# Kernel tuning notes

Measured on AMD Instinct MI355X. Metric: run time of the kernel, lower is better.

Reference implementation:

```python
import jax, jax.numpy as jnp
import numpy as np

B, H, SEQLEN, HEAD_DIM = 1, 16, 4096, 64
SCALE = 1.0 / float(np.sqrt(HEAD_DIM))


def setup_inputs() -> dict:
    key = jax.random.key(0)
    kq, kk, kv = jax.random.split(key, 3)
    q = jax.random.normal(kq, (B, H, SEQLEN, HEAD_DIM), dtype=jnp.float32)
    k = jax.random.normal(kk, (B, H, HEAD_DIM, SEQLEN), dtype=jnp.float32)  # pre-transposed
    v = jax.random.normal(kv, (B, H, SEQLEN, HEAD_DIM), dtype=jnp.float32)
    return {"q": q, "k": k, "v": v}


def reference(q, k, v):
    # causal additive mask: -inf strictly above the diagonal
    mask = jnp.where(
        jnp.triu(jnp.ones((SEQLEN, SEQLEN), dtype=bool), k=1),
        jnp.float32(-jnp.inf), jnp.float32(0.0),
    ).astype(q.dtype)
    scores = jnp.einsum('bhsd,bhdt->bhst', q, k) * SCALE + mask  # [B,H,S,S]
    row_max = jnp.max(scores, axis=-1, keepdims=True)
    p_exp = jnp.exp(scores - row_max)
    denom = jnp.sum(p_exp, axis=-1, keepdims=True)
    p = p_exp / denom                                            # softmax probs
    out = jnp.einsum('bhst,bhtd->bhsd', p, v)                    # [B,H,S,D]
    row_sum = jnp.sum(p, axis=2)                                 # per-key accumulated attention [B,H,S]
    return (out, row_sum)
```

## Files before the change

kernel.cpp:

```cpp
#include <hip/hip_runtime.h>
#include <hip/hip_bf16.h>

#define HEADS 16
#define SEQ   4096
#define DIM   64
#define QT    64
#define KT    64
#define SCALE 0.125f
#define CF    0.18033688011112042f
#define LOG2E 1.4426950408889634f

typedef __bf16 v8bf  __attribute__((ext_vector_type(8)));
typedef __bf16 v4bf  __attribute__((ext_vector_type(4)));
typedef float  f32x4 __attribute__((ext_vector_type(4)));

__device__ __forceinline__ __bf16 to_bf(float f) { return (__bf16)f; }
__device__ __forceinline__ float ex2(float x) { return __builtin_amdgcn_exp2f(x); }
__device__ __forceinline__ float lg2(float x) { return __builtin_amdgcn_logf(x); }

__device__ __forceinline__ void gload16(const __bf16* g, __bf16* l) {
    __builtin_amdgcn_global_load_lds(
        (const __attribute__((address_space(1))) void*)g,
        (__attribute__((address_space(3))) void*)l,
        16, 0, 0);
}

__global__ __launch_bounds__(256) void conv_q_kernel(
    const float* __restrict__ qg, __bf16* __restrict__ Qb)
{
    size_t i = ((size_t)blockIdx.x * 256 + threadIdx.x) * 8;
    float4 f0 = *(const float4*)(qg + i);
    float4 f1 = *(const float4*)(qg + i + 4);
    v8bf o;
    o[0] = to_bf(f0.x * CF); o[1] = to_bf(f0.y * CF);
    o[2] = to_bf(f0.z * CF); o[3] = to_bf(f0.w * CF);
    o[4] = to_bf(f1.x * CF); o[5] = to_bf(f1.y * CF);
    o[6] = to_bf(f1.z * CF); o[7] = to_bf(f1.w * CF);
    *(v8bf*)(Qb + i) = o;
}

__global__ __launch_bounds__(256) void conv_kv_kernel(
    const float* __restrict__ kg, const float* __restrict__ vg,
    __bf16* __restrict__ Kb, __bf16* __restrict__ Vb)
{
    __shared__ __bf16 ldsT[64][65];
    const int h   = blockIdx.y;
    const int t0  = blockIdx.x * 64;
    const int tid = threadIdx.x;
    const int rr  = tid >> 2;
    const int cq  = (tid & 3) * 16;

    if (blockIdx.z == 0) {
        const float* src = kg + ((size_t)h * DIM + rr) * SEQ + t0 + cq;
        #pragma unroll
        for (int j = 0; j < 4; ++j) {
            float4 f = *(const float4*)(src + 4 * j);
            ldsT[rr][cq + 4 * j + 0] = to_bf(f.x);
            ldsT[rr][cq + 4 * j + 1] = to_bf(f.y);
            ldsT[rr][cq + 4 * j + 2] = to_bf(f.z);
            ldsT[rr][cq + 4 * j + 3] = to_bf(f.w);
        }
        __syncthreads();
        __bf16* dst = Kb + (size_t)h * SEQ * DIM + (size_t)(t0 + rr) * DIM + cq;
        v8bf o0, o1;
        #pragma unroll
        for (int i = 0; i < 8; ++i) {
            o0[i] = ldsT[cq + i][rr];
            o1[i] = ldsT[cq + 8 + i][rr];
        }
        *(v8bf*)dst = o0;
        *(v8bf*)(dst + 8) = o1;
    } else {
        const float* src = vg + ((size_t)h * SEQ + t0 + rr) * DIM + cq;
        #pragma unroll
        for (int j = 0; j < 4; ++j) {
            float4 f = *(const float4*)(src + 4 * j);
            ldsT[rr][cq + 4 * j + 0] = to_bf(f.x);
            ldsT[rr][cq + 4 * j + 1] = to_bf(f.y);
            ldsT[rr][cq + 4 * j + 2] = to_bf(f.z);
            ldsT[rr][cq + 4 * j + 3] = to_bf(f.w);
        }
        __syncthreads();
        __bf16* dst0 = Vb + ((size_t)h * DIM + rr) * SEQ + t0;
        const int n  = cq >> 4;
        const int c0 = 32 * (n >> 1) + 4 * (n & 1);
        #pragma unroll
        for (int j2 = 0; j2 < 4; ++j2) {
            v4bf ch;
            #pragma unroll
            for (int r = 0; r < 4; ++r)
                ch[r] = ldsT[cq + 4 * j2 + r][rr];
            *(v4bf*)(dst0 + c0 + 8 * j2) = ch;
        }
    }
}

__global__ __launch_bounds__(256, 2) void fa_fwd2_kernel(
    const __bf16* __restrict__ Qb, const __bf16* __restrict__ Kb,
    const __bf16* __restrict__ Vb, float* __restrict__ outg,
    float* __restrict__ lseg)
{
    const int b    = blockIdx.x;
    const int xcd  = b & 7;
    const int j    = b >> 3;
    const int h    = 2 * xcd + (j & 1);
    const int bq   = j >> 1;
    const int tid  = threadIdx.x;
    const int wave = tid >> 6;
    const int lane = tid & 63;
    const int g    = lane >> 4;
    const int l16  = lane & 15;

    __shared__ alignas(16) __bf16 ldsK[2][2][KT * DIM];
    __shared__ alignas(16) __bf16 ldsV[2][2][DIM * KT];

    const int r0 = tid >> 3;
    const int c0 = tid & 7;
    const size_t kOff0 = (size_t)r0 * DIM + (size_t)((c0 ^ (r0 & 7)) << 3);
    const size_t kOff1 = (size_t)(r0 + 32) * DIM + (size_t)((c0 ^ ((r0 + 32) & 7)) << 3);
    const size_t vOff0 = (size_t)r0 * SEQ + (size_t)((c0 ^ (r0 & 7)) << 3);
    const size_t vOff1 = (size_t)(r0 + 32) * SEQ + (size_t)((c0 ^ ((r0 + 32) & 7)) << 3);
    const __bf16* KbH = Kb + (size_t)h * SEQ * DIM;
    const __bf16* VbH = Vb + (size_t)h * DIM * SEQ;
    const int ldsW = wave * 512;

    #pragma unroll 1
    for (int pi = 0; pi < 2; ++pi) {
        const int qtile = pi ? (63 - bq) : bq;
        const int qw = qtile * QT + wave * 16;
        const int nt  = qtile + 1;
        const int nIt = (nt + 1) >> 1;
        const int q   = qw + l16;

        const __bf16* qrow = Qb + ((size_t)h * SEQ + q) * DIM + g * 8;
        v8bf aq0 = *(const v8bf*)qrow;
        v8bf aq1 = *(const v8bf*)(qrow + 32);

        f32x4 acc[4];
        #pragma unroll
        for (int n = 0; n < 4; ++n) acc[n] = (f32x4){0.f, 0.f, 0.f, 0.f};
        float lp[4] = {0.f, 0.f, 0.f, 0.f};

        int cur = 0;
        #pragma unroll
        for (int u = 0; u < 2; ++u) {
            const __bf16* kb = KbH + (size_t)(64 * u) * DIM;
            const __bf16* vb = VbH + 64 * u;
            gload16(kb + kOff0, &ldsK[0][u][ldsW]);
            gload16(kb + kOff1, &ldsK[0][u][2048 + ldsW]);
            gload16(vb + vOff0, &ldsV[0][u][ldsW]);
            gload16(vb + vOff1, &ldsV[0][u][2048 + ldsW]);
        }
        __syncthreads();

        #pragma unroll 1
        for (int it = 0; it < nIt; ++it) {
            if (it + 1 < nIt) {
                #pragma unroll
                for (int u = 0; u < 2; ++u) {
                    const __bf16* kb = KbH + (size_t)(128 * (it + 1) + 64 * u) * DIM;
                    const __bf16* vb = VbH + 128 * (it + 1) + 64 * u;
                    gload16(kb + kOff0, &ldsK[cur ^ 1][u][ldsW]);
                    gload16(kb + kOff1, &ldsK[cur ^ 1][u][2048 + ldsW]);
                    gload16(vb + vOff0, &ldsV[cur ^ 1][u][ldsW]);
                    gload16(vb + vOff1, &ldsV[cur ^ 1][u][2048 + ldsW]);
                }
            }
            f32x4 s0[4], s1[4];
            #pragma unroll
            for (int n = 0; n < 4; ++n) {
                s0[n] = (f32x4){0.f, 0.f, 0.f, 0.f};
                s1[n] = (f32x4){0.f, 0.f, 0.f, 0.f};
            }
            __builtin_amdgcn_s_setprio(1);
            #pragma unroll
            for (int kk = 0; kk < 2; ++kk) {
                #pragma unroll
                for (int n = 0; n < 4; ++n) {
                    int row  = 16 * n + l16;
                    int byte = row * 128 + kk * 64 + g * 16;
                    byte ^= (row & 7) << 4;
                    v8bf ak0 = *(const v8bf*)&ldsK[cur][0][byte >> 1];
                    v8bf ak1 = *(const v8bf*)&ldsK[cur][1][byte >> 1];
                    s0[n] = __builtin_amdgcn_mfma_f32_16x16x32_bf16(
                        ak0, kk ? aq1 : aq0, s0[n], 0, 0, 0);
                    s1[n] = __builtin_amdgcn_mfma_f32_16x16x32_bf16(
                        ak1, kk ? aq1 : aq0, s1[n], 0, 0, 0);
                }
            }
            __builtin_amdgcn_s_setprio(0);
            const int st0 = 2 * it, st1 = 2 * it + 1;
            if (st0 >= nt - 1) {
                const int lim = (qtile - st0) * 64 + wave * 16 + l16;
                #pragma unroll
                for (int n = 0; n < 4; ++n)
                    #pragma unroll
                    for (int r = 0; r < 4; ++r)
                        if (16 * n + 4 * g + r > lim) s0[n][r] = -3.0e38f;
            }
            if (st1 >= nt - 1) {
                const int lim = (qtile - st1) * 64 + wave * 16 + l16;
                #pragma unroll
                for (int n = 0; n < 4; ++n)
                    #pragma unroll
                    for (int r = 0; r < 4; ++r)
                        if (16 * n + 4 * g + r > lim) s1[n][r] = -3.0e38f;
            }
            v8bf pa00, pa01, pa10, pa11;
            #pragma unroll
            for (int n = 0; n < 4; ++n) {
                #pragma unroll
                for (int r = 0; r < 4; ++r) {
                    float p0 = ex2(s0[n][r]);
                    float p1 = ex2(s1[n][r]);
                    lp[r] += p0 + p1;
                    if (n < 2) { pa00[(n & 1) * 4 + r] = to_bf(p0);
                                 pa10[(n & 1) * 4 + r] = to_bf(p1); }
                    else       { pa01[(n & 1) * 4 + r] = to_bf(p0);
                                 pa11[(n & 1) * 4 + r] = to_bf(p1); }
                }
            }
            __builtin_amdgcn_s_setprio(1);
            #pragma unroll
            for (int kk = 0; kk < 2; ++kk) {
                #pragma unroll
                for (int n = 0; n < 4; ++n) {
                    int row  = 16 * n + l16;
                    int byte = row * 128 + kk * 64 + g * 16;
                    byte ^= (row & 7) << 4;
                    v8bf av0 = *(const v8bf*)&ldsV[cur][0][byte >> 1];
                    v8bf av1 = *(const v8bf*)&ldsV[cur][1][byte >> 1];
                    acc[n] = __builtin_amdgcn_mfma_f32_16x16x32_bf16(
                        av0, kk ? pa01 : pa00, acc[n], 0, 0, 0);
                    acc[n] = __builtin_amdgcn_mfma_f32_16x16x32_bf16(
                        av1, kk ? pa11 : pa10, acc[n], 0, 0, 0);
                }
            }
            __builtin_amdgcn_s_setprio(0);
            __syncthreads();
            cur ^= 1;
        }

        float l = (lp[0] + lp[1]) + (lp[2] + lp[3]);
        l += __shfl_xor(l, 16);
        l += __shfl_xor(l, 32);
        const float inv = 1.0f / l;
        float* orow = outg + ((size_t)h * SEQ + q) * DIM;
        #pragma unroll
        for (int n = 0; n < 4; ++n) {
            f32x4 o = acc[n];
            o[0] *= inv; o[1] *= inv; o[2] *= inv; o[3] *= inv;
            *(f32x4*)(orow + 16 * n + 4 * g) = o;
        }
        if (g == 0)
            lseg[h * SEQ + q] = lg2(l);
    }
}

__global__ __launch_bounds__(256, 2) void fa_colsum2_kernel(
    const __bf16* __restrict__ Qb, const __bf16* __restrict__ Kb,
    const float* __restrict__ lseg, float* __restrict__ rsg)
{
    const int b    = blockIdx.x;
    const int xcd  = b & 7;
    const int j    = b >> 3;
    const int h    = 2 * xcd + (j & 1);
    const int ta   = j >> 1;
    const int tb   = 63 - ta;
    const int tid  = threadIdx.x;
    const int wave = tid >> 6;
    const int lane = tid & 63;
    const int g    = lane >> 4;
    const int l16  = lane & 15;

    __shared__ alignas(16) __bf16 ldsK2[2][KT * DIM];
    __shared__ float cs[2][4][KT];

    const int r0 = tid >> 3;
    const int c0 = tid & 7;
    const size_t kOff0 = (size_t)r0 * DIM + (size_t)((c0 ^ (r0 & 7)) << 3);
    const size_t kOff1 = (size_t)(r0 + 32) * DIM + (size_t)((c0 ^ ((r0 + 32) & 7)) << 3);
    const __bf16* KbH = Kb + (size_t)h * SEQ * DIM;
    const int ldsW = wave * 512;

    gload16(KbH + (size_t)ta * KT * DIM + kOff0, &ldsK2[0][ldsW]);
    gload16(KbH + (size_t)ta * KT * DIM + kOff1, &ldsK2[0][2048 + ldsW]);
    gload16(KbH + (size_t)tb * KT * DIM + kOff0, &ldsK2[1][ldsW]);
    gload16(KbH + (size_t)tb * KT * DIM + kOff1, &ldsK2[1][2048 + ldsW]);
    __syncthreads();

    float accA[4] = {0.f, 0.f, 0.f, 0.f};
    float accB[4] = {0.f, 0.f, 0.f, 0.f};

    #pragma unroll 1
    for (int qt = ta; qt < SEQ / QT; ++qt) {
        const int qw = qt * QT + wave * 16;
        const __bf16* qrow = Qb + ((size_t)h * SEQ + qw + l16) * DIM + g * 8;
        v8bf aq0 = *(const v8bf*)qrow;
        v8bf aq1 = *(const v8bf*)(qrow + 32);
        float4 lse4 = *(const float4*)(lseg + (size_t)h * SEQ + qw + 4 * g);

        {
            f32x4 s[4];
            #pragma unroll
            for (int n = 0; n < 4; ++n) s[n] = (f32x4){0.f, 0.f, 0.f, 0.f};
            __builtin_amdgcn_s_setprio(1);
            #pragma unroll
            for (int kk = 0; kk < 2; ++kk)
                #pragma unroll
                for (int n = 0; n < 4; ++n) {
                    int row  = 16 * n + l16;
                    int byte = row * 128 + kk * 64 + g * 16;
                    byte ^= (row & 7) << 4;
                    v8bf bk = *(const v8bf*)&ldsK2[0][byte >> 1];
                    s[n] = __builtin_amdgcn_mfma_f32_16x16x32_bf16(
                        kk ? aq1 : aq0, bk, s[n], 0, 0, 0);
                }
            __builtin_amdgcn_s_setprio(0);
            if (qt == ta) {
                #pragma unroll
                for (int n = 0; n < 4; ++n) {
                    const int key = ta * KT + 16 * n + l16;
                    #pragma unroll
                    for (int r = 0; r < 4; ++r) {
                        float e = ex2(s[n][r] - lse4[r]);
                        accA[n] += (key <= qw + 4 * g + r) ? e : 0.f;
                    }
                }
            } else {
                #pragma unroll
                for (int n = 0; n < 4; ++n)
                    #pragma unroll
                    for (int r = 0; r < 4; ++r)
                        accA[n] += ex2(s[n][r] - lse4[r]);
            }
        }
        if (qt >= tb) {
            f32x4 s[4];
            #pragma unroll
            for (int n = 0; n < 4; ++n) s[n] = (f32x4){0.f, 0.f, 0.f, 0.f};
            __builtin_amdgcn_s_setprio(1);
            #pragma unroll
            for (int kk = 0; kk < 2; ++kk)
                #pragma unroll
                for (int n = 0; n < 4; ++n) {
                    int row  = 16 * n + l16;
                    int byte = row * 128 + kk * 64 + g * 16;
                    byte ^= (row & 7) << 4;
                    v8bf bk = *(const v8bf*)&ldsK2[1][byte >> 1];
                    s[n] = __builtin_amdgcn_mfma_f32_16x16x32_bf16(
                        kk ? aq1 : aq0, bk, s[n], 0, 0, 0);
                }
            __builtin_amdgcn_s_setprio(0);
            if (qt == tb) {
                #pragma unroll
                for (int n = 0; n < 4; ++n) {
                    const int key = tb * KT + 16 * n + l16;
                    #pragma unroll
                    for (int r = 0; r < 4; ++r) {
                        float e = ex2(s[n][r] - lse4[r]);
                        accB[n] += (key <= qw + 4 * g + r) ? e : 0.f;
                    }
                }
            } else {
                #pragma unroll
                for (int n = 0; n < 4; ++n)
                    #pragma unroll
                    for (int r = 0; r < 4; ++r)
                        accB[n] += ex2(s[n][r] - lse4[r]);
            }
        }
    }

    #pragma unroll
    for (int n = 0; n < 4; ++n) {
        accA[n] += __shfl_xor(accA[n], 16);
        accA[n] += __shfl_xor(accA[n], 32);
        accB[n] += __shfl_xor(accB[n], 16);
        accB[n] += __shfl_xor(accB[n], 32);
    }
    if (lane < 16) {
        #pragma unroll
        for (int n = 0; n < 4; ++n) {
            cs[0][wave][16 * n + lane] = accA[n];
            cs[1][wave][16 * n + lane] = accB[n];
        }
    }
    __syncthreads();
    if (tid < KT) {
        rsg[(size_t)h * SEQ + ta * KT + tid] =
            cs[0][0][tid] + cs[0][1][tid] + cs[0][2][tid] + cs[0][3][tid];
    } else if (tid < 2 * KT) {
        const int t = tid - KT;
        rsg[(size_t)h * SEQ + tb * KT + t] =
            cs[1][0][t] + cs[1][1][t] + cs[1][2][t] + cs[1][3][t];
    }
}

__global__ __launch_bounds__(256, 1) void fa_fwd_v1_kernel(
    const float* __restrict__ qg, const float* __restrict__ kg,
    const float* __restrict__ vg, float* __restrict__ outg,
    float* __restrict__ lseg)
{
    const int h    = blockIdx.y;
    const int q0   = blockIdx.x * QT;
    const int tid  = threadIdx.x;
    const int wave = tid >> 6;
    const int lane = tid & 63;
    const int g    = lane >> 4;
    const int l16  = lane & 15;

    __shared__ alignas(16) __bf16 ldsK[KT * DIM];
    __shared__ alignas(16) __bf16 ldsV[DIM * KT];
    __shared__ alignas(16) __bf16 ldsP[4][16 * 72];

    const int qw = q0 + wave * 16;
    v8bf aq[2];
    {
        const float* qrow = qg + ((size_t)h * SEQ + qw + l16) * DIM;
        #pragma unroll
        for (int kk = 0; kk < 2; ++kk) {
            const float* p = qrow + kk * 32 + g * 8;
            float4 f0 = *(const float4*)p;
            float4 f1 = *(const float4*)(p + 4);
            aq[kk][0] = to_bf(f0.x); aq[kk][1] = to_bf(f0.y);
            aq[kk][2] = to_bf(f0.z); aq[kk][3] = to_bf(f0.w);
            aq[kk][4] = to_bf(f1.x); aq[kk][5] = to_bf(f1.y);
            aq[kk][6] = to_bf(f1.z); aq[kk][7] = to_bf(f1.w);
        }
    }
    f32x4 acc[4];
    #pragma unroll
    for (int n = 0; n < 4; ++n) acc[n] = (f32x4){0.f, 0.f, 0.f, 0.f};
    float m_r[4], l_r[4];
    #pragma unroll
    for (int r = 0; r < 4; ++r) { m_r[r] = -__builtin_inff(); l_r[r] = 0.f; }

    const int ntiles = q0 / KT + 1;
    const int kd = tid >> 2;
    const int kc = (tid & 3) * 16;

    for (int t = 0; t < ntiles; ++t) {
        const int t0 = t * KT;
        __syncthreads();
        {
            const float* src = kg + ((size_t)h * DIM + kd) * SEQ + t0 + kc;
            #pragma unroll
            for (int j = 0; j < 4; ++j) {
                float4 f = *(const float4*)(src + 4 * j);
                #pragma unroll
                for (int i = 0; i < 4; ++i) {
                    int row  = kc + 4 * j + i;
                    int byte = row * 128 + kd * 2;
                    byte ^= (row & 7) << 4;
                    ldsK[byte >> 1] = to_bf(((const float*)&f)[i]);
                }
            }
        }
        {
            const float* src = vg + ((size_t)h * SEQ + t0 + kd) * DIM + kc;
            #pragma unroll
            for (int j = 0; j < 4; ++j) {
                float4 f = *(const float4*)(src + 4 * j);
                #pragma unroll
                for (int i = 0; i < 4; ++i) {
                    int row  = kc + 4 * j + i;
                    int byte = row * 128 + kd * 2;
                    byte ^= (row & 7) << 4;
                    ldsV[byte >> 1] = to_bf(((const float*)&f)[i]);
                }
            }
        }
        __syncthreads();

        f32x4 s[4];
        #pragma unroll
        for (int n = 0; n < 4; ++n) s[n] = (f32x4){0.f, 0.f, 0.f, 0.f};
        #pragma unroll
        for (int kk = 0; kk < 2; ++kk)
            #pragma unroll
            for (int n = 0; n < 4; ++n) {
                int row  = 16 * n + l16;
                int byte = row * 128 + kk * 64 + g * 16;
                byte ^= (row & 7) << 4;
                v8bf bk = *(const v8bf*)&ldsK[byte >> 1];
                s[n] = __builtin_amdgcn_mfma_f32_16x16x32_bf16(aq[kk], bk, s[n], 0, 0, 0);
            }
        float pvv[4][4];
        #pragma unroll
        for (int r = 0; r < 4; ++r) {
            const int qq = qw + 4 * g + r;
            float sv[4];
            #pragma unroll
            for (int n = 0; n < 4; ++n) {
                int key = t0 + 16 * n + l16;
                sv[n] = (key <= qq) ? s[n][r] * (SCALE * LOG2E) : -3.0e38f;
            }
            float mx = fmaxf(fmaxf(sv[0], sv[1]), fmaxf(sv[2], sv[3]));
            mx = fmaxf(mx, __shfl_xor(mx, 1));
            mx = fmaxf(mx, __shfl_xor(mx, 2));
            mx = fmaxf(mx, __shfl_xor(mx, 4));
            mx = fmaxf(mx, __shfl_xor(mx, 8));
            float mnew = fmaxf(m_r[r], mx);
            float corr = ex2(m_r[r] - mnew);
            m_r[r] = mnew;
            float rs = 0.f;
            #pragma unroll
            for (int n = 0; n < 4; ++n) {
                float p = (sv[n] > -1.0e38f) ? ex2(sv[n] - mnew) : 0.f;
                pvv[n][r] = p;
                rs += p;
            }
            rs += __shfl_xor(rs, 1);
            rs += __shfl_xor(rs, 2);
            rs += __shfl_xor(rs, 4);
            rs += __shfl_xor(rs, 8);
            l_r[r] = l_r[r] * corr + rs;
            #pragma unroll
            for (int n = 0; n < 4; ++n) acc[n][r] *= corr;
        }
        #pragma unroll
        for (int n = 0; n < 4; ++n)
            #pragma unroll
            for (int r = 0; r < 4; ++r)
                ldsP[wave][(4 * g + r) * 72 + 16 * n + l16] = to_bf(pvv[n][r]);
        asm volatile("s_waitcnt lgkmcnt(0)" ::: "memory");
        __builtin_amdgcn_sched_barrier(0);
        #pragma unroll
        for (int kk = 0; kk < 2; ++kk) {
            v8bf ap = *(const v8bf*)&ldsP[wave][l16 * 72 + 32 * kk + 8 * g];
            #pragma unroll
            for (int n = 0; n < 4; ++n) {
                int row  = 16 * n + l16;
                int byte = row * 128 + kk * 64 + g * 16;
                byte ^= (row & 7) << 4;
                v8bf bv = *(const v8bf*)&ldsV[byte >> 1];
                acc[n] = __builtin_amdgcn_mfma_f32_16x16x32_bf16(ap, bv, acc[n], 0, 0, 0);
            }
        }
    }
    #pragma unroll
    for (int r = 0; r < 4; ++r) {
        const int qq  = qw + 4 * g + r;
        const float inv = 1.0f / l_r[r];
        float* orow = outg + ((size_t)h * SEQ + qq) * DIM;
        #pragma unroll
        for (int n = 0; n < 4; ++n)
            orow[16 * n + l16] = acc[n][r] * inv;
        if (l16 == 0)
            lseg[h * SEQ + qq] = m_r[r] + lg2(l_r[r]);
    }
}

__global__ __launch_bounds__(256, 1) void fa_colsum_v1_kernel(
    const float* __restrict__ qg, const float* __restrict__ kg,
    const float* __restrict__ lseg, float* __restrict__ rsg)
{
    const int h    = blockIdx.y;
    const int t0   = blockIdx.x * KT;
    const int tid  = threadIdx.x;
    const int wave = tid >> 6;
    const int lane = tid & 63;
    const int g    = lane >> 4;
    const int l16  = lane & 15;

    __shared__ alignas(16) __bf16 ldsK[KT * DIM];
    __shared__ float cs[4][KT];
    {
        const int kd = tid >> 2;
        const int kc = (tid & 3) * 16;
        const float* src = kg + ((size_t)h * DIM + kd) * SEQ + t0 + kc;
        #pragma unroll
        for (int j = 0; j < 4; ++j) {
            float4 f = *(const float4*)(src + 4 * j);
            #pragma unroll
            for (int i = 0; i < 4; ++i) {
                int row  = kc + 4 * j + i;
                int byte = row * 128 + kd * 2;
                byte ^= (row & 7) << 4;
                ldsK[byte >> 1] = to_bf(((const float*)&f)[i]);
            }
        }
    }
    __syncthreads();
    float colacc[4] = {0.f, 0.f, 0.f, 0.f};
    for (int qt = t0 / QT; qt < SEQ / QT; ++qt) {
        const int qw = qt * QT + wave * 16;
        const float* qrow = qg + ((size_t)h * SEQ + qw + l16) * DIM;
        v8bf aq[2];
        #pragma unroll
        for (int kk = 0; kk < 2; ++kk) {
            const float* p = qrow + kk * 32 + g * 8;
            float4 f0 = *(const float4*)p;
            float4 f1 = *(const float4*)(p + 4);
            aq[kk][0] = to_bf(f0.x); aq[kk][1] = to_bf(f0.y);
            aq[kk][2] = to_bf(f0.z); aq[kk][3] = to_bf(f0.w);
            aq[kk][4] = to_bf(f1.x); aq[kk][5] = to_bf(f1.y);
            aq[kk][6] = to_bf(f1.z); aq[kk][7] = to_bf(f1.w);
        }
        float lse_r[4];
        #pragma unroll
        for (int r = 0; r < 4; ++r)
            lse_r[r] = lseg[h * SEQ + qw + 4 * g + r];
        f32x4 s[4];
        #pragma unroll
        for (int n = 0; n < 4; ++n) s[n] = (f32x4){0.f, 0.f, 0.f, 0.f};
        #pragma unroll
        for (int kk = 0; kk < 2; ++kk)
            #pragma unroll
            for (int n = 0; n < 4; ++n) {
                int row  = 16 * n + l16;
                int byte = row * 128 + kk * 64 + g * 16;
                byte ^= (row & 7) << 4;
                v8bf bk = *(const v8bf*)&ldsK[byte >> 1];
                s[n] = __builtin_amdgcn_mfma_f32_16x16x32_bf16(aq[kk], bk, s[n], 0, 0, 0);
            }
        #pragma unroll
        for (int n = 0; n < 4; ++n) {
            const int key = t0 + 16 * n + l16;
            #pragma unroll
            for (int r = 0; r < 4; ++r) {
                const int qq = qw + 4 * g + r;
                if (key <= qq)
                    colacc[n] += ex2(s[n][r] * (SCALE * LOG2E) - lse_r[r]);
            }
        }
    }
    #pragma unroll
    for (int n = 0; n < 4; ++n) {
        colacc[n] += __shfl_xor(colacc[n], 16);
        colacc[n] += __shfl_xor(colacc[n], 32);
    }
    if (lane < 16) {
        #pragma unroll
        for (int n = 0; n < 4; ++n)
            cs[wave][16 * n + lane] = colacc[n];
    }
    __syncthreads();
    if (tid < KT) {
        float v = cs[0][tid] + cs[1][tid] + cs[2][tid] + cs[3][tid];
        rsg[h * SEQ + t0 + tid] = v;
    }
}

extern "C" void kernel_launch(void* const* d_in, const int* in_sizes, int n_in,
                              void* d_out, int out_size, void* d_ws, size_t ws_size,
                              hipStream_t stream) {
    (void)in_sizes; (void)n_in; (void)out_size;
    const float* qg = (const float*)d_in[0];
    const float* kg = (const float*)d_in[1];
    const float* vg = (const float*)d_in[2];
    float* outg = (float*)d_out;
    float* rsg  = outg + (size_t)HEADS * SEQ * DIM;

    const size_t nElem   = (size_t)HEADS * SEQ * DIM;
    const size_t lseB    = (size_t)HEADS * SEQ * sizeof(float);
    const size_t needB   = lseB + 3 * nElem * sizeof(__bf16);

    if (ws_size >= needB) {
        float*  lseg = (float*)d_ws;
        __bf16* Qb = (__bf16*)((char*)d_ws + lseB);
        __bf16* Kb = Qb + nElem;
        __bf16* Vb = Kb + nElem;
        conv_q_kernel<<<dim3((int)(nElem / 2048)), 256, 0, stream>>>(qg, Qb);
        conv_kv_kernel<<<dim3(SEQ / 64, HEADS, 2), 256, 0, stream>>>(kg, vg, Kb, Vb);
        fa_fwd2_kernel<<<dim3(512), 256, 0, stream>>>(Qb, Kb, Vb, outg, lseg);
        fa_colsum2_kernel<<<dim3(512), 256, 0, stream>>>(Qb, Kb, lseg, rsg);
    } else {
        float* lseg = (float*)d_ws;
        dim3 grid(SEQ / QT, HEADS);
        fa_fwd_v1_kernel<<<grid, 256, 0, stream>>>(qg, kg, vg, outg, lseg);
        fa_colsum_v1_kernel<<<grid, 256, 0, stream>>>(qg, kg, lseg, rsg);
    }
}
```

Baseline: 105.3 us.

## Fuse paired query tiles over shared K/V loop and split column-sum work

```diff
diff --git a/kernel.cpp b/kernel.cpp
--- a/kernel.cpp
+++ b/kernel.cpp
@@ -104,12 +104,17 @@
     const int xcd  = b & 7;
     const int j    = b >> 3;
     const int h    = 2 * xcd + (j & 1);
-    const int bq   = j >> 1;
+    const int a    = j >> 1;
     const int tid  = threadIdx.x;
     const int wave = tid >> 6;
     const int lane = tid & 63;
     const int g    = lane >> 4;
     const int l16  = lane & 15;
+    const int wit  = wave * 16 + l16;
+
+    const int na  = a + 1;
+    const int nb  = 64 - a;
+    const int nIt = (nb + 1) >> 1;
 
     __shared__ alignas(16) __bf16 ldsK[2][2][KT * DIM];
     __shared__ alignas(16) __bf16 ldsV[2][2][DIM * KT];
@@ -124,149 +129,219 @@
     const __bf16* VbH = Vb + (size_t)h * DIM * SEQ;
     const int ldsW = wave * 512;
 
+    const int qlo = a * QT + wit;
+    const int qhi = (63 - a) * QT + wit;
+
+    const __bf16* qlr = Qb + ((size_t)h * SEQ + qlo) * DIM + g * 8;
+    const __bf16* qhr = Qb + ((size_t)h * SEQ + qhi) * DIM + g * 8;
+    v8bf aqlo0 = *(const v8bf*)qlr;
+    v8bf aqlo1 = *(const v8bf*)(qlr + 32);
+    v8bf aqhi0 = *(const v8bf*)qhr;
+    v8bf aqhi1 = *(const v8bf*)(qhr + 32);
+
+    f32x4 accl[4], acch[4];
+    #pragma unroll
+    for (int n = 0; n < 4; ++n) {
+        accl[n] = (f32x4){0.f, 0.f, 0.f, 0.f};
+        acch[n] = (f32x4){0.f, 0.f, 0.f, 0.f};
+    }
+    float lpl[4] = {0.f, 0.f, 0.f, 0.f};
+    float lph[4] = {0.f, 0.f, 0.f, 0.f};
+
+    int cur = 0;
+    #pragma unroll
+    for (int u = 0; u < 2; ++u) {
+        const __bf16* kb = KbH + (size_t)(64 * u) * DIM;
+        const __bf16* vb = VbH + 64 * u;
+        gload16(kb + kOff0, &ldsK[0][u][ldsW]);
+        gload16(kb + kOff1, &ldsK[0][u][2048 + ldsW]);
+        gload16(vb + vOff0, &ldsV[0][u][ldsW]);
+        gload16(vb + vOff1, &ldsV[0][u][2048 + ldsW]);
+    }
+    __syncthreads();
+
+    auto sub_full = [&](int u, int t) {
+        f32x4 sl[4], sh[4];
+        #pragma unroll
+        for (int n = 0; n < 4; ++n) {
+            sl[n] = (f32x4){0.f, 0.f, 0.f, 0.f};
+            sh[n] = (f32x4){0.f, 0.f, 0.f, 0.f};
+        }
+        __builtin_amdgcn_s_setprio(1);
+        #pragma unroll
+        for (int kk = 0; kk < 2; ++kk) {
+            #pragma unroll
+            for (int n = 0; n < 4; ++n) {
+                int row  = 16 * n + l16;
+                int byte = row * 128 + kk * 64 + g * 16;
+                byte ^= (row & 7) << 4;
+                v8bf ak = *(const v8bf*)&ldsK[cur][u][byte >> 1];
+                sl[n] = __builtin_amdgcn_mfma_f32_16x16x32_bf16(
+                    ak, kk ? aqlo1 : aqlo0, sl[n], 0, 0, 0);
+                sh[n] = __builtin_amdgcn_mfma_f32_16x16x32_bf16(
+                    ak, kk ? aqhi1 : aqhi0, sh[n], 0, 0, 0);
+            }
+        }
+        __builtin_amdgcn_s_setprio(0);
+        if (t >= na - 1) {
+            const int lim = (a - t) * 64 + wit;
+            #pragma unroll
+            for (int n = 0; n < 4; ++n)
+                #pragma unroll
+                for (int r = 0; r < 4; ++r)
+                    if (16 * n + 4 * g + r > lim) sl[n][r] = -3.0e38f;
+        }
+        v8bf pl0, pl1, ph0, ph1;
+        #pragma unroll
+        for (int n = 0; n < 4; ++n) {
+            #pragma unroll
+            for (int r = 0; r < 4; ++r) {
+                float p = ex2(sl[n][r]);
+                float q = ex2(sh[n][r]);
+                lpl[r] += p;
+                lph[r] += q;
+                if (n < 2) { pl0[(n & 1) * 4 + r] = to_bf(p);
+                             ph0[(n & 1) * 4 + r] = to_bf(q); }
+                else       { pl1[(n & 1) * 4 + r] = to_bf(p);
+                             ph1[(n & 1) * 4 + r] = to_bf(q); }
+            }
+        }
+        __builtin_amdgcn_s_setprio(1);
+        #pragma unroll
+        for (int kk = 0; kk < 2; ++kk) {
+            #pragma unroll
+            for (int n = 0; n < 4; ++n) {
+                int row  = 16 * n + l16;
+                int byte = row * 128 + kk * 64 + g * 16;
+                byte ^= (row & 7) << 4;
+                v8bf av = *(const v8bf*)&ldsV[cur][u][byte >> 1];
+                accl[n] = __builtin_amdgcn_mfma_f32_16x16x32_bf16(
+                    av, kk ? pl1 : pl0, accl[n], 0, 0, 0);
+                acch[n] = __builtin_amdgcn_mfma_f32_16x16x32_bf16(
+                    av, kk ? ph1 : ph0, acch[n], 0, 0, 0);
+            }
+        }
+        __builtin_amdgcn_s_setprio(0);
+    };
+
+    auto sub_hi = [&](int u, int t) {
+        f32x4 sh[4];
+        #pragma unroll
+        for (int n = 0; n < 4; ++n) sh[n] = (f32x4){0.f, 0.f, 0.f, 0.f};
+        __builtin_amdgcn_s_setprio(1);
+        #pragma unroll
+        for (int kk = 0; kk < 2; ++kk) {
+            #pragma unroll
+            for (int n = 0; n < 4; ++n) {
+                int row  = 16 * n + l16;
+                int byte = row * 128 + kk * 64 + g * 16;
+                byte ^= (row & 7) << 4;
+                v8bf ak = *(const v8bf*)&ldsK[cur][u][byte >> 1];
+                sh[n] = __builtin_amdgcn_mfma_f32_16x16x32_bf16(
+                    ak, kk ? aqhi1 : aqhi0, sh[n], 0, 0, 0);
+            }
+        }
+        __builtin_amdgcn_s_setprio(0);
+        if (t >= nb - 1) {
+            const int lim = (63 - a - t) * 64 + wit;
+            #pragma unroll
+            for (int n = 0; n < 4; ++n)
+                #pragma unroll
+                for (int r = 0; r < 4; ++r)
+                    if (16 * n + 4 * g + r > lim) sh[n][r] = -3.0e38f;
+        }
+        v8bf ph0, ph1;
+        #pragma unroll
+        for (int n = 0; n < 4; ++n) {
+            #pragma unroll
+            for (int r = 0; r < 4; ++r) {
+                float q = ex2(sh[n][r]);
+                lph[r] += q;
+                if (n < 2) ph0[(n & 1) * 4 + r] = to_bf(q);
+                else       ph1[(n & 1) * 4 + r] = to_bf(q);
+            }
+        }
+        __builtin_amdgcn_s_setprio(1);
+        #pragma unroll
+        for (int kk = 0; kk < 2; ++kk) {
+            #pragma unroll
+            for (int n = 0; n < 4; ++n) {
+                int row  = 16 * n + l16;
+                int byte = row * 128 + kk * 64 + g * 16;
+                byte ^= (row & 7) << 4;
+                v8bf av = *(const v8bf*)&ldsV[cur][u][byte >> 1];
+                acch[n] = __builtin_amdgcn_mfma_f32_16x16x32_bf16(
+                    av, kk ? ph1 : ph0, acch[n], 0, 0, 0);
+            }
+        }
+        __builtin_amdgcn_s_setprio(0);
+    };
+
     #pragma unroll 1
-    for (int pi = 0; pi < 2; ++pi) {
-        const int qtile = pi ? (63 - bq) : bq;
-        const int qw = qtile * QT + wave * 16;
-        const int nt  = qtile + 1;
-        const int nIt = (nt + 1) >> 1;
-        const int q   = qw + l16;
-
-        const __bf16* qrow = Qb + ((size_t)h * SEQ + q) * DIM + g * 8;
-        v8bf aq0 = *(const v8bf*)qrow;
-        v8bf aq1 = *(const v8bf*)(qrow + 32);
-
-        f32x4 acc[4];
-        #pragma unroll
-        for (int n = 0; n < 4; ++n) acc[n] = (f32x4){0.f, 0.f, 0.f, 0.f};
-        float lp[4] = {0.f, 0.f, 0.f, 0.f};
-
-        int cur = 0;
-        #pragma unroll
-        for (int u = 0; u < 2; ++u) {
-            const __bf16* kb = KbH + (size_t)(64 * u) * DIM;
-            const __bf16* vb = VbH + 64 * u;
-            gload16(kb + kOff0, &ldsK[0][u][ldsW]);
-            gload16(kb + kOff1, &ldsK[0][u][2048 + ldsW]);
-            gload16(vb + vOff0, &ldsV[0][u][ldsW]);
-            gload16(vb + vOff1, &ldsV[0][u][2048 + ldsW]);
-        }
+    for (int it = 0; it < nIt; ++it) {
+        if (it + 1 < nIt) {
+            #pragma unroll
+            for (int u = 0; u < 2; ++u) {
+                const __bf16* kb = KbH + (size_t)(128 * (it + 1) + 64 * u) * DIM;
+                const __bf16* vb = VbH + 128 * (it + 1) + 64 * u;
+                gload16(kb + kOff0, &ldsK[cur ^ 1][u][ldsW]);
+                gload16(kb + kOff1, &ldsK[cur ^ 1][u][2048 + ldsW]);
+                gload16(vb + vOff0, &ldsV[cur ^ 1][u][ldsW]);
+                gload16(vb + vOff1, &ldsV[cur ^ 1][u][2048 + ldsW]);
+            }
+        }
+        const int t0 = 2 * it;
+        if (t0 < na) { sub_full(0, t0); sub_full(1, t0 + 1); }
+        else         { sub_hi(0, t0);   sub_hi(1, t0 + 1);   }
         __syncthreads();
-
-        #pragma unroll 1
-        for (int it = 0; it < nIt; ++it) {
-            if (it + 1 < nIt) {
-                #pragma unroll
-                for (int u = 0; u < 2; ++u) {
-                    const __bf16* kb = KbH + (size_t)(128 * (it + 1) + 64 * u) * DIM;
-                    const __bf16* vb = VbH + 128 * (it + 1) + 64 * u;
-                    gload16(kb + kOff0, &ldsK[cur ^ 1][u][ldsW]);
-                    gload16(kb + kOff1, &ldsK[cur ^ 1][u][2048 + ldsW]);
-                    gload16(vb + vOff0, &ldsV[cur ^ 1][u][ldsW]);
-                    gload16(vb + vOff1, &ldsV[cur ^ 1][u][2048 + ldsW]);
-                }
-            }
-            f32x4 s0[4], s1[4];
-            #pragma unroll
-            for (int n = 0; n < 4; ++n) {
-                s0[n] = (f32x4){0.f, 0.f, 0.f, 0.f};
-                s1[n] = (f32x4){0.f, 0.f, 0.f, 0.f};
-            }
-            __builtin_amdgcn_s_setprio(1);
-            #pragma unroll
-            for (int kk = 0; kk < 2; ++kk) {
-                #pragma unroll
-                for (int n = 0; n < 4; ++n) {
-                    int row  = 16 * n + l16;
-                    int byte = row * 128 + kk * 64 + g * 16;
-                    byte ^= (row & 7) << 4;
-                    v8bf ak0 = *(const v8bf*)&ldsK[cur][0][byte >> 1];
-                    v8bf ak1 = *(const v8bf*)&ldsK[cur][1][byte >> 1];
-                    s0[n] = __builtin_amdgcn_mfma_f32_16x16x32_bf16(
-                        ak0, kk ? aq1 : aq0, s0[n], 0, 0, 0);
-                    s1[n] = __builtin_amdgcn_mfma_f32_16x16x32_bf16(
-                        ak1, kk ? aq1 : aq0, s1[n], 0, 0, 0);
-                }
-            }
-            __builtin_amdgcn_s_setprio(0);
-            const int st0 = 2 * it, st1 = 2 * it + 1;
-            if (st0 >= nt - 1) {
-                const int lim = (qtile - st0) * 64 + wave * 16 + l16;
-                #pragma unroll
-                for (int n = 0; n < 4; ++n)
-                    #pragma unroll
-                    for (int r = 0; r < 4; ++r)
-                        if (16 * n + 4 * g + r > lim) s0[n][r] = -3.0e38f;
-            }
-            if (st1 >= nt - 1) {
-                const int lim = (qtile - st1) * 64 + wave * 16 + l16;
-                #pragma unroll
-                for (int n = 0; n < 4; ++n)
-                    #pragma unroll
-                    for (int r = 0; r < 4; ++r)
-                        if (16 * n + 4 * g + r > lim) s1[n][r] = -3.0e38f;
-            }
-            v8bf pa00, pa01, pa10, pa11;
-            #pragma unroll
-            for (int n = 0; n < 4; ++n) {
-                #pragma unroll
-                for (int r = 0; r < 4; ++r) {
-                    float p0 = ex2(s0[n][r]);
-                    float p1 = ex2(s1[n][r]);
-                    lp[r] += p0 + p1;
-                    if (n < 2) { pa00[(n & 1) * 4 + r] = to_bf(p0);
-                                 pa10[(n & 1) * 4 + r] = to_bf(p1); }
-                    else       { pa01[(n & 1) * 4 + r] = to_bf(p0);
-                                 pa11[(n & 1) * 4 + r] = to_bf(p1); }
-                }
-            }
-            __builtin_amdgcn_s_setprio(1);
-            #pragma unroll
-            for (int kk = 0; kk < 2; ++kk) {
-                #pragma unroll
-                for (int n = 0; n < 4; ++n) {
-                    int row  = 16 * n + l16;
-                    int byte = row * 128 + kk * 64 + g * 16;
-                    byte ^= (row & 7) << 4;
-                    v8bf av0 = *(const v8bf*)&ldsV[cur][0][byte >> 1];
-                    v8bf av1 = *(const v8bf*)&ldsV[cur][1][byte >> 1];
-                    acc[n] = __builtin_amdgcn_mfma_f32_16x16x32_bf16(
-                        av0, kk ? pa01 : pa00, acc[n], 0, 0, 0);
-                    acc[n] = __builtin_amdgcn_mfma_f32_16x16x32_bf16(
-                        av1, kk ? pa11 : pa10, acc[n], 0, 0, 0);
-                }
-            }
-            __builtin_amdgcn_s_setprio(0);
-            __syncthreads();
-            cur ^= 1;
-        }
-
-        float l = (lp[0] + lp[1]) + (lp[2] + lp[3]);
+        cur ^= 1;
+    }
+
+    {
+        float l = (lpl[0] + lpl[1]) + (lpl[2] + lpl[3]);
         l += __shfl_xor(l, 16);
         l += __shfl_xor(l, 32);
         const float inv = 1.0f / l;
-        float* orow = outg + ((size_t)h * SEQ + q) * DIM;
+        float* orow = outg + ((size_t)h * SEQ + qlo) * DIM;
         #pragma unroll
         for (int n = 0; n < 4; ++n) {
-            f32x4 o = acc[n];
+            f32x4 o = accl[n];
             o[0] *= inv; o[1] *= inv; o[2] *= inv; o[3] *= inv;
             *(f32x4*)(orow + 16 * n + 4 * g) = o;
         }
-        if (g == 0)
-            lseg[h * SEQ + q] = lg2(l);
-    }
-}
-
-__global__ __launch_bounds__(256, 2) void fa_colsum2_kernel(
+        if (g == 0) lseg[h * SEQ + qlo] = lg2(l);
+    }
+    {
+        float l = (lph[0] + lph[1]) + (lph[2] + lph[3]);
+        l += __shfl_xor(l, 16);
+        l += __shfl_xor(l, 32);
+        const float inv = 1.0f / l;
+        float* orow = outg + ((size_t)h * SEQ + qhi) * DIM;
+        #pragma unroll
+        for (int n = 0; n < 4; ++n) {
+            f32x4 o = acch[n];
+            o[0] *= inv; o[1] *= inv; o[2] *= inv; o[3] *= inv;
+            *(f32x4*)(orow + 16 * n + 4 * g) = o;
+        }
+        if (g == 0) lseg[h * SEQ + qhi] = lg2(l);
+    }
+}
+
+__global__ __launch_bounds__(256, 4) void fa_colsum2_kernel(
     const __bf16* __restrict__ Qb, const __bf16* __restrict__ Kb,
-    const float* __restrict__ lseg, float* __restrict__ rsg)
+    const float* __restrict__ lseg, float* __restrict__ partg)
 {
     const int b    = blockIdx.x;
     const int xcd  = b & 7;
     const int j    = b >> 3;
     const int h    = 2 * xcd + (j & 1);
-    const int ta   = j >> 1;
+    const int m    = j >> 1;
+    const int ta   = m & 31;
+    const int half = m >> 5;
     const int tb   = 63 - ta;
+    const int smid = (ta <= 15) ? (ta + 33) : 48;
+    const int qlo  = half ? smid : ta;
+    const int qhiE = half ? 64 : smid;
     const int tid  = threadIdx.x;
     const int wave = tid >> 6;
     const int lane = tid & 63;
@@ -293,7 +368,7 @@
     float accB[4] = {0.f, 0.f, 0.f, 0.f};
 
     #pragma unroll 1
-    for (int qt = ta; qt < SEQ / QT; ++qt) {
+    for (int qt = qlo; qt < qhiE; ++qt) {
         const int qw = qt * QT + wave * 16;
         const __bf16* qrow = Qb + ((size_t)h * SEQ + qw + l16) * DIM + g * 8;
         v8bf aq0 = *(const v8bf*)qrow;
@@ -387,14 +462,25 @@
         }
     }
     __syncthreads();
+    float* pg = partg + (size_t)half * HEADS * SEQ + (size_t)h * SEQ;
     if (tid < KT) {
-        rsg[(size_t)h * SEQ + ta * KT + tid] =
+        pg[ta * KT + tid] =
             cs[0][0][tid] + cs[0][1][tid] + cs[0][2][tid] + cs[0][3][tid];
     } else if (tid < 2 * KT) {
         const int t = tid - KT;
-        rsg[(size_t)h * SEQ + tb * KT + t] =
+        pg[tb * KT + t] =
             cs[1][0][t] + cs[1][1][t] + cs[1][2][t] + cs[1][3][t];
     }
+}
+
+__global__ __launch_bounds__(256) void rs_add_kernel(
+    const float* __restrict__ partg, float* __restrict__ rsg)
+{
+    const int i = blockIdx.x * 256 + threadIdx.x;
+    f32x4 x = *(const f32x4*)(partg + (size_t)i * 4);
+    f32x4 y = *(const f32x4*)(partg + (size_t)HEADS * SEQ + (size_t)i * 4);
+    x[0] += y[0]; x[1] += y[1]; x[2] += y[2]; x[3] += y[3];
+    *(f32x4*)(rsg + (size_t)i * 4) = x;
 }
 
 __global__ __launch_bounds__(256, 1) void fa_fwd_v1_kernel(
@@ -662,10 +748,12 @@
         __bf16* Qb = (__bf16*)((char*)d_ws + lseB);
         __bf16* Kb = Qb + nElem;
         __bf16* Vb = Kb + nElem;
+        float* partg = (float*)Vb;
         conv_q_kernel<<<dim3((int)(nElem / 2048)), 256, 0, stream>>>(qg, Qb);
         conv_kv_kernel<<<dim3(SEQ / 64, HEADS, 2), 256, 0, stream>>>(kg, vg, Kb, Vb);
         fa_fwd2_kernel<<<dim3(512), 256, 0, stream>>>(Qb, Kb, Vb, outg, lseg);
-        fa_colsum2_kernel<<<dim3(512), 256, 0, stream>>>(Qb, Kb, lseg, rsg);
+        fa_colsum2_kernel<<<dim3(1024), 256, 0, stream>>>(Qb, Kb, lseg, partg);
+        rs_add_kernel<<<dim3(HEADS * SEQ / 1024), 256, 0, stream>>>(partg, rsg);
     } else {
         float* lseg = (float*)d_ws;
         dim3 grid(SEQ / QT, HEADS);
```

Measured after the change: 106.3 us. No clear change (+0.9%).
